# Kernel tuning notes

Hardware: AMD Instinct MI355X
Metric: run time of the kernel (lower is better)

Reference implementation:

```python
import jax, jax.numpy as jnp
import numpy as np
from jax import lax

DIM = 2048
NUM_HEADS = 16
HEAD_DIM = DIM // NUM_HEADS  # 128
BLOCK = 128
EPS = 1e-6


def setup_inputs() -> dict:
    key = jax.random.key(0)
    kq, kk, kv = jax.random.split(key, 3)
    B, S = 2, 4096
    q = jax.random.normal(kq, (B, S, DIM), dtype=jnp.float32)
    k = jax.random.normal(kk, (B, S, DIM), dtype=jnp.float32)
    v = jax.random.normal(kv, (B, S, DIM), dtype=jnp.float32)
    return {"q": q, "k": k, "v": v}


def _flash_attn(q, k, v):
    # q,k,v: [B, S, DIM] -> [B, H, S, Dh]
    B, S, _ = q.shape
    def split_heads(x):
        return jnp.transpose(x.reshape(B, -1, NUM_HEADS, HEAD_DIM), (0, 2, 1, 3))
    scale = HEAD_DIM ** (-0.5)
    qh = split_heads(q) * scale  # pre-scale, as in original __call__
    kh = split_heads(k)
    vh = split_heads(v)
    Sk = kh.shape[2]
    num_chunks = (Sk + BLOCK - 1) // BLOCK

    o0 = jnp.zeros((B, NUM_HEADS, S, HEAD_DIM), dtype=jnp.float32)
    l0 = jnp.zeros((B, NUM_HEADS, S, 1), dtype=jnp.float32)
    m0 = jnp.full((B, NUM_HEADS, S, 1), -jnp.inf, dtype=jnp.float32)

    def chunk_scanner(carry, chunk_idx):
        o, l, m_run = carry
        start = chunk_idx * BLOCK
        k_c = lax.dynamic_slice(kh, (0, 0, start, 0), (B, NUM_HEADS, BLOCK, HEAD_DIM))
        v_c = lax.dynamic_slice(vh, (0, 0, start, 0), (B, NUM_HEADS, BLOCK, HEAD_DIM))
        # scores: [B, H, Sq, BLOCK]; note second division by sqrt(head_dim) (faithful)
        s = jnp.einsum('bhqd,bhkd->bhqk', qh, k_c,
                       precision=lax.Precision.HIGHEST) / jnp.sqrt(jnp.float32(HEAD_DIM))
        m_chunk = jnp.max(s, axis=-1, keepdims=True)
        m_new = jnp.maximum(m_run, m_chunk)
        exp_scale = jnp.exp(m_run - m_new)
        exp_s = jnp.exp(s - m_chunk)  # faithful: uses m_chunk, not m_new
        l_new = l * exp_scale + jnp.sum(exp_s, axis=-1, keepdims=True)
        o_chunk = jnp.einsum('bhqk,bhkd->bhqd', exp_s, v_c,
                             precision=lax.Precision.HIGHEST)
        o_new = o * exp_scale + o_chunk
        return (o_new, l_new, m_new), None

    (o, l, _), _ = lax.scan(chunk_scanner, (o0, l0, m0), jnp.arange(num_chunks))
    o = o / (l + EPS)
    out = jnp.transpose(o, (0, 2, 1, 3)).reshape(B, -1, DIM)
    return out


def reference(q, k, v):
    return _flash_attn(q, k, v)
```

## Files before the change

kernel.cpp:

```cpp
#include <hip/hip_runtime.h>
#include <hip/hip_bf16.h>
#include <stdint.h>

#define SEQ     4096
#define DMODEL  2048
#define NHEADS  16
#define DHEAD   128
#define QBLK    256
#define CHUNK   128
#define NCHUNK  (SEQ / CHUNK)

typedef __bf16 bf16_t;
typedef bf16_t bf16x8 __attribute__((ext_vector_type(8)));
typedef bf16_t bf16x4 __attribute__((ext_vector_type(4)));
typedef float  f32x4  __attribute__((ext_vector_type(4)));

typedef __attribute__((address_space(3))) uint32_t       lds_u32_t;
typedef __attribute__((address_space(1))) const uint32_t glb_u32_t;

static __device__ __forceinline__ void gload16(const void* g, void* l) {
  __builtin_amdgcn_global_load_lds((glb_u32_t*)g, (lds_u32_t*)l, 16, 0, 0);
}

static __device__ __forceinline__ float exp2_fast(float x) {
  float r;
  asm("v_exp_f32 %0, %1\n\ts_nop 0" : "=v"(r) : "v"(x));
  return r;
}

__device__ __forceinline__ uint32_t swz(int row, int colbyte) {
  return ((uint32_t)(row * 256 + colbyte)) ^ ((uint32_t)(row & 15) << 4);
}

__global__ __launch_bounds__(256)
void prep_k(const float* __restrict__ kk, bf16_t* __restrict__ kb) {
  const size_t e = ((size_t)blockIdx.x * 256 + threadIdx.x) * 8;
  const int dm = (int)(e % DMODEL);
  const int s  = (int)((e / DMODEL) % SEQ);
  const int b  = (int)(e / ((size_t)DMODEL * SEQ));
  float4 x0 = *(const float4*)(kk + e);
  float4 x1 = *(const float4*)(kk + e + 4);
  bf16x8 y;
  y[0]=(bf16_t)x0.x; y[1]=(bf16_t)x0.y; y[2]=(bf16_t)x0.z; y[3]=(bf16_t)x0.w;
  y[4]=(bf16_t)x1.x; y[5]=(bf16_t)x1.y; y[6]=(bf16_t)x1.z; y[7]=(bf16_t)x1.w;
  const size_t out = (((size_t)(b * NHEADS + (dm >> 7)) * SEQ + s) << 7) + (dm & 127);
  *(bf16x8*)(kb + out) = y;
}

__global__ __launch_bounds__(256)
void prep_v(const float* __restrict__ vv, bf16_t* __restrict__ vb) {
  __shared__ bf16_t T[128 * 132];
  const int t = threadIdx.x;
  const int s0 = blockIdx.x * 128, h = blockIdx.y, b = blockIdx.z;
  const float* src = vv + ((size_t)(b * SEQ + s0)) * DMODEL + h * DHEAD;
#pragma unroll
  for (int p = 0; p < 16; ++p) {
    const int sr = p * 8 + (t >> 5), c4 = (t & 31) * 4;
    float4 x = *(const float4*)(src + (size_t)sr * DMODEL + c4);
    bf16_t* d = T + sr * 132 + c4;
    d[0]=(bf16_t)x.x; d[1]=(bf16_t)x.y; d[2]=(bf16_t)x.z; d[3]=(bf16_t)x.w;
  }
  __syncthreads();
  bf16_t* out = vb + ((size_t)(b * NHEADS + h)) * DHEAD * SEQ;
#pragma unroll
  for (int p = 0; p < 8; ++p) {
    const int d = p * 16 + (t >> 4), sc8 = (t & 15) * 8;
    bf16x8 y;
#pragma unroll
    for (int j = 0; j < 8; ++j) y[j] = T[(sc8 + j) * 132 + d];
    *(bf16x8*)(out + (size_t)d * SEQ + s0 + sc8) = y;
  }
}

__global__ __launch_bounds__(512, 1)
void fa_fwd_p(const float* __restrict__ qg, const bf16_t* __restrict__ kbg,
              const bf16_t* __restrict__ vbg, float* __restrict__ og)
{
  __shared__ char smem[65536];

  const int tid  = threadIdx.x;
  const int wave = tid >> 6;
  const int lane = tid & 63;
  const int l15  = lane & 15;
  const int lhi  = lane >> 4;

  const int nwg = gridDim.x * gridDim.y * gridDim.z;
  const int lin = blockIdx.x + gridDim.x * (blockIdx.y + gridDim.y * blockIdx.z);
  const int wg  = (lin % 8) * (nwg / 8) + lin / 8;
  const int bx  = wg % gridDim.x;
  const int h   = (wg / gridDim.x) % NHEADS;
  const int b   = wg / (gridDim.x * NHEADS);
  const int bh  = b * NHEADS + h;
  const int qrow0 = bx * QBLK + wave * 32;

  const bf16_t* kcb = kbg + ((size_t)bh * SEQ) * DHEAD;
  const bf16_t* vcb = vbg + ((size_t)bh * DHEAD) * SEQ;

#define ISSUE_K(koff, key0)                                                    \
  {                                                                            \
    _Pragma("unroll")                                                          \
    for (int u = 0; u < 2; ++u) {                                              \
      const int row = u * 32 + wave * 4 + (lane >> 4);                         \
      const int gx  = (row & 3) | (((row >> 3) & 3) << 2);                     \
      gload16(kcb + (size_t)((key0) + row) * 128 + (((lane & 15) ^ gx) * 8),   \
              smem + (koff) + u * 8192 + wave * 1024);                         \
    }                                                                          \
  }
#define ISSUE_V(key0)                                                          \
  {                                                                            \
    _Pragma("unroll")                                                          \
    for (int u = 0; u < 4; ++u) {                                              \
      const int dh = u * 32 + wave * 4 + (lane >> 4);                          \
      gload16(vcb + (size_t)dh * SEQ + (key0) + (((lane & 15) ^ (dh & 15)) * 8),\
              smem + 32768 + u * 8192 + wave * 1024);                          \
    }                                                                          \
  }

  ISSUE_K(0, 0);
  ISSUE_K(16384, 64);
  ISSUE_V(0);

  bf16x8 qa[8];
  {
    const float sc = 1.4426950408889634f / 128.0f;
#pragma unroll
    for (int h2 = 0; h2 < 2; ++h2) {
      const float* qp =
          qg + ((size_t)(b * SEQ + qrow0 + h2 * 16 + l15)) * DMODEL + h * DHEAD;
#pragma unroll
      for (int kb = 0; kb < 4; ++kb) {
        const float* p8 = qp + kb * 32 + lhi * 8;
        float4 x0 = *(const float4*)p8;
        float4 x1 = *(const float4*)(p8 + 4);
        bf16x8 a;
        a[0] = (bf16_t)(x0.x * sc); a[1] = (bf16_t)(x0.y * sc);
        a[2] = (bf16_t)(x0.z * sc); a[3] = (bf16_t)(x0.w * sc);
        a[4] = (bf16_t)(x1.x * sc); a[5] = (bf16_t)(x1.y * sc);
        a[6] = (bf16_t)(x1.z * sc); a[7] = (bf16_t)(x1.w * sc);
        qa[h2 * 4 + kb] = a;
      }
    }
  }

  f32x4 oacc[16];
#pragma unroll
  for (int nt = 0; nt < 16; ++nt) { f32x4 z = {0.f,0.f,0.f,0.f}; oacc[nt] = z; }
  float m_run0 = -INFINITY, l_run0 = 0.f;
  float m_run1 = -INFINITY, l_run1 = 0.f;

  asm volatile("s_waitcnt vmcnt(4)\n\ts_barrier" ::: "memory");

  for (int c = 0; c < NCHUNK; ++c) {
    f32x4 s0[8], s1[8];
    __builtin_amdgcn_s_setprio(1);
#pragma unroll
    for (int t = 0; t < 2; ++t) {
      const char* Kt = smem + t * 16384;
#pragma unroll
      for (int nl = 0; nl < 4; ++nl) {
        const int rowA = (nl >> 1) * 32 + (l15 >> 2) * 8 + (nl & 1) * 4 + (l15 & 3);
        const int gx   = (rowA & 3) | (((rowA >> 3) & 3) << 2);
        f32x4 a0 = {0.f, 0.f, 0.f, 0.f};
        f32x4 a1 = {0.f, 0.f, 0.f, 0.f};
#pragma unroll
        for (int j = 0; j < 4; ++j) {
          const uint32_t byte = (uint32_t)(rowA * 256) + ((j * 64 + lhi * 16) ^ (gx << 4));
          bf16x8 kf = *(const bf16x8*)(Kt + byte);
          a0 = __builtin_amdgcn_mfma_f32_16x16x32_bf16(kf, qa[j], a0, 0, 0, 0);
          a1 = __builtin_amdgcn_mfma_f32_16x16x32_bf16(kf, qa[4 + j], a1, 0, 0, 0);
        }
        s0[t * 4 + nl] = a0;
        s1[t * 4 + nl] = a1;
      }
    }
    __builtin_amdgcn_s_setprio(0);

    asm volatile("s_waitcnt vmcnt(0) lgkmcnt(0)\n\ts_barrier" ::: "memory");
    if (c + 1 < NCHUNK) {
      ISSUE_K(0, (c + 1) * CHUNK);
      ISSUE_K(16384, (c + 1) * CHUNK + 64);
    }

    bf16x8 pa0[4], pa1[4];
#define SOFTMAX_HALF(SA, PA, MRUN, LRUN, OBASE)                                \
    {                                                                          \
      float mc = SA[0][0];                                                     \
      _Pragma("unroll")                                                        \
      for (int i = 0; i < 8; ++i)                                              \
        _Pragma("unroll")                                                      \
        for (int r = 0; r < 4; ++r)                                            \
          if (i + r) mc = fmaxf(mc, SA[i][r]);                                 \
      mc = fmaxf(mc, __shfl_xor(mc, 16, 64));                                  \
      mc = fmaxf(mc, __shfl_xor(mc, 32, 64));                                  \
      const bool skip = __all(mc <= MRUN);                                     \
      const float mn = fmaxf(MRUN, mc);                                        \
      const float e  = exp2_fast(MRUN - mn);                                   \
      MRUN = mn;                                                               \
      float ps = 0.f;                                                          \
      _Pragma("unroll")                                                        \
      for (int nt = 0; nt < 8; ++nt)                                           \
        _Pragma("unroll")                                                      \
        for (int r = 0; r < 4; ++r) {                                          \
          const float p = exp2_fast(SA[nt][r] - mc);                           \
          ps += p;                                                             \
          PA[(nt >> 2) * 2 + ((nt >> 1) & 1)][(nt & 1) * 4 + r] = (bf16_t)p;   \
        }                                                                      \
      ps += __shfl_xor(ps, 16, 64);                                            \
      ps += __shfl_xor(ps, 32, 64);                                            \
      if (skip) {                                                              \
        LRUN += ps;                                                            \
      } else {                                                                 \
        LRUN = LRUN * e + ps;                                                  \
        _Pragma("unroll")                                                      \
        for (int r = 0; r < 4; ++r) {                                          \
          const float er = __shfl(e, lhi * 4 + r, 16);                         \
          _Pragma("unroll")                                                    \
          for (int nt = 0; nt < 8; ++nt) oacc[(OBASE) + nt][r] *= er;          \
        }                                                                      \
      }                                                                        \
    }
    SOFTMAX_HALF(s0, pa0, m_run0, l_run0, 0)
    SOFTMAX_HALF(s1, pa1, m_run1, l_run1, 8)
#undef SOFTMAX_HALF

    __builtin_amdgcn_s_setprio(1);
#pragma unroll
    for (int kv = 0; kv < 4; ++kv) {
#pragma unroll
      for (int nt = 0; nt < 8; ++nt) {
        const int dh = nt * 16 + l15;
        const uint32_t byte = (uint32_t)(32768 + dh * 256) +
            (((uint32_t)(kv * 64 + lhi * 16)) ^ ((dh & 15) << 4));
        bf16x8 vf = *(const bf16x8*)(smem + byte);
        oacc[nt]     = __builtin_amdgcn_mfma_f32_16x16x32_bf16(pa0[kv], vf, oacc[nt], 0, 0, 0);
        oacc[8 + nt] = __builtin_amdgcn_mfma_f32_16x16x32_bf16(pa1[kv], vf, oacc[8 + nt], 0, 0, 0);
      }
    }
    __builtin_amdgcn_s_setprio(0);

    asm volatile("s_waitcnt vmcnt(0) lgkmcnt(0)\n\ts_barrier" ::: "memory");
    if (c + 1 < NCHUNK) ISSUE_V((c + 1) * CHUNK);
  }

  {
    char* Ow = smem + wave * 8192;
#pragma unroll
    for (int h2 = 0; h2 < 2; ++h2) {
      const float lrl = h2 ? l_run1 : l_run0;
      float lr[4];
#pragma unroll
      for (int r = 0; r < 4; ++r) lr[r] = __shfl(lrl, lhi * 4 + r, 16);
#pragma unroll
      for (int nt = 0; nt < 8; ++nt)
#pragma unroll
        for (int r = 0; r < 4; ++r) {
          const int row = lhi * 4 + r;
          const int colb = (nt * 16 + l15) * 4;
          *(float*)(Ow + row * 512 + (colb ^ ((row & 7) << 4))) =
              oacc[h2 * 8 + nt][r] / (lr[r] + 1e-6f);
        }
      asm volatile("s_waitcnt lgkmcnt(0)" ::: "memory");
      __builtin_amdgcn_sched_barrier(0);
#pragma unroll
      for (int p = 0; p < 8; ++p) {
        const int row = p * 2 + (lane >> 5);
        const int colb = (lane & 31) * 16;
        f32x4 val = *(const f32x4*)(Ow + row * 512 + (colb ^ ((row & 7) << 4)));
        *(f32x4*)((char*)(og + ((size_t)(b * SEQ + qrow0 + h2 * 16 + row)) * DMODEL +
                          h * DHEAD) + colb) = val;
      }
      asm volatile("s_waitcnt lgkmcnt(0)" ::: "memory");
      __builtin_amdgcn_sched_barrier(0);
    }
  }
#undef ISSUE_K
#undef ISSUE_V
}

__global__ __launch_bounds__(512, 2)
void fa_fwd_raw(const float* __restrict__ qg, const float* __restrict__ kg,
                const float* __restrict__ vg, float* __restrict__ og)
{
  __shared__ bf16_t Kl[CHUNK * DHEAD];
  __shared__ bf16_t Vt[DHEAD * CHUNK];
  const int tid = threadIdx.x, wave = tid >> 6, lane = tid & 63;
  const int l15 = lane & 15, lhi = lane >> 4;
  const int b = blockIdx.z, h = blockIdx.y;
  const int qrow0 = blockIdx.x * 128 + wave * 16;
  bf16x8 qa[4];
  {
    const float* qp = qg + ((size_t)(b * SEQ + qrow0 + l15)) * DMODEL + h * DHEAD;
    const float sc = 1.0f / 128.0f;
#pragma unroll
    for (int kb = 0; kb < 4; ++kb) {
      const float* p8 = qp + kb * 32 + lhi * 8;
      float4 x0 = *(const float4*)p8; float4 x1 = *(const float4*)(p8 + 4);
      bf16x8 a;
      a[0]=(bf16_t)(x0.x*sc); a[1]=(bf16_t)(x0.y*sc); a[2]=(bf16_t)(x0.z*sc); a[3]=(bf16_t)(x0.w*sc);
      a[4]=(bf16_t)(x1.x*sc); a[5]=(bf16_t)(x1.y*sc); a[6]=(bf16_t)(x1.z*sc); a[7]=(bf16_t)(x1.w*sc);
      qa[kb] = a;
    }
  }
  f32x4 oacc[8];
#pragma unroll
  for (int nt = 0; nt < 8; ++nt) { f32x4 z = {0.f,0.f,0.f,0.f}; oacc[nt] = z; }
  float m_run[4] = {-INFINITY,-INFINITY,-INFINITY,-INFINITY};
  float l_run[4] = {0.f,0.f,0.f,0.f};
  const float* kbp = kg + ((size_t)b * SEQ) * DMODEL + h * DHEAD;
  const float* vbp = vg + ((size_t)b * SEQ) * DMODEL + h * DHEAD;
  const int krow16 = tid >> 5, kc4 = (tid & 31) * 4;
  const int vdh = tid & 127, vkg = (tid >> 7) * 8;
  for (int c = 0; c < NCHUNK; ++c) {
    const int key0 = c * CHUNK;
#pragma unroll
    for (int pass = 0; pass < 8; ++pass) {
      const int key = pass * 16 + krow16;
      const float4 x = *(const float4*)(kbp + (size_t)(key0 + key) * DMODEL + kc4);
      bf16x4 y; y[0]=(bf16_t)x.x; y[1]=(bf16_t)x.y; y[2]=(bf16_t)x.z; y[3]=(bf16_t)x.w;
      *(bf16x4*)((char*)Kl + swz(key, kc4 * 2)) = y;
    }
#pragma unroll
    for (int it = 0; it < 4; ++it) {
      const int kb0 = it * 32 + vkg;
      const float* vp = vbp + (size_t)(key0 + kb0) * DMODEL + vdh;
      bf16x8 y;
#pragma unroll
      for (int j = 0; j < 8; ++j) y[j] = (bf16_t)vp[(size_t)j * DMODEL];
      *(bf16x8*)((char*)Vt + swz(vdh, kb0 * 2)) = y;
    }
    __syncthreads();
    f32x4 sacc[8];
#pragma unroll
    for (int nt = 0; nt < 8; ++nt) {
      f32x4 acc = {0.f,0.f,0.f,0.f};
      const int key = nt * 16 + l15;
#pragma unroll
      for (int kb = 0; kb < 4; ++kb) {
        bf16x8 bfr = *(const bf16x8*)((const char*)Kl + swz(key, (kb*32+lhi*8)*2));
        acc = __builtin_amdgcn_mfma_f32_16x16x32_bf16(qa[kb], bfr, acc, 0, 0, 0);
      }
      sacc[nt] = acc;
    }
    __syncthreads();
    float mc[4];
#pragma unroll
    for (int r = 0; r < 4; ++r) {
      float m0 = sacc[0][r];
#pragma unroll
      for (int nt = 1; nt < 8; ++nt) m0 = fmaxf(m0, sacc[nt][r]);
      mc[r] = m0;
    }
#pragma unroll
    for (int sh = 1; sh < 16; sh <<= 1)
#pragma unroll
      for (int r = 0; r < 4; ++r) mc[r] = fmaxf(mc[r], __shfl_xor(mc[r], sh, 64));
    float esc[4], psum[4];
#pragma unroll
    for (int r = 0; r < 4; ++r) {
      const float mn = fmaxf(m_run[r], mc[r]);
      esc[r] = __expf(m_run[r] - mn); m_run[r] = mn; psum[r] = 0.f;
    }
    bf16_t* Pw = Kl + wave * (16 * 128);
#pragma unroll
    for (int nt = 0; nt < 8; ++nt)
#pragma unroll
      for (int r = 0; r < 4; ++r) {
        const float p = __expf(sacc[nt][r] - mc[r]);
        psum[r] += p;
        const int row = lhi * 4 + r;
        *(bf16_t*)((char*)Pw + swz(row, (nt*16+l15)*2)) = (bf16_t)p;
      }
#pragma unroll
    for (int sh = 1; sh < 16; sh <<= 1)
#pragma unroll
      for (int r = 0; r < 4; ++r) psum[r] += __shfl_xor(psum[r], sh, 64);
#pragma unroll
    for (int r = 0; r < 4; ++r) l_run[r] = l_run[r] * esc[r] + psum[r];
#pragma unroll
    for (int nt = 0; nt < 8; ++nt) {
      f32x4 o = oacc[nt];
      o[0]*=esc[0]; o[1]*=esc[1]; o[2]*=esc[2]; o[3]*=esc[3];
      oacc[nt] = o;
    }
    asm volatile("s_waitcnt lgkmcnt(0)" ::: "memory");
    __builtin_amdgcn_sched_barrier(0);
#pragma unroll
    for (int kb = 0; kb < 4; ++kb) {
      bf16x8 pf = *(const bf16x8*)((const char*)Pw + swz(l15, (kb*32+lhi*8)*2));
#pragma unroll
      for (int nt = 0; nt < 8; ++nt) {
        const int dh = nt * 16 + l15;
        bf16x8 vf = *(const bf16x8*)((const char*)Vt + swz(dh, (kb*32+lhi*8)*2));
        oacc[nt] = __builtin_amdgcn_mfma_f32_16x16x32_bf16(pf, vf, oacc[nt], 0, 0, 0);
      }
    }
    __syncthreads();
  }
#pragma unroll
  for (int nt = 0; nt < 8; ++nt)
#pragma unroll
    for (int r = 0; r < 4; ++r) {
      const int row = lhi * 4 + r;
      og[((size_t)(b * SEQ + qrow0 + row)) * DMODEL + h * DHEAD + nt * 16 + l15] =
          oacc[nt][r] / (l_run[r] + 1e-6f);
    }
}

extern "C" void kernel_launch(void* const* d_in, const int* in_sizes, int n_in,
                              void* d_out, int out_size, void* d_ws, size_t ws_size,
                              hipStream_t stream) {
  const float* q = (const float*)d_in[0];
  const float* k = (const float*)d_in[1];
  const float* v = (const float*)d_in[2];
  float* o = (float*)d_out;
  const int B = in_sizes[0] / (SEQ * DMODEL);
  const size_t kv_bytes = (size_t)B * NHEADS * SEQ * DHEAD * 2;
  if (ws_size >= 2 * kv_bytes) {
    bf16_t* kb = (bf16_t*)d_ws;
    bf16_t* vb = (bf16_t*)((char*)d_ws + kv_bytes);
    const int nthr = (int)(((size_t)B * SEQ * DMODEL) / 8);
    prep_k<<<nthr / 256, 256, 0, stream>>>(k, kb);
    dim3 gv(SEQ / 128, NHEADS, B);
    prep_v<<<gv, 256, 0, stream>>>(v, vb);
    dim3 grid(SEQ / QBLK, NHEADS, B);
    fa_fwd_p<<<grid, 512, 0, stream>>>(q, kb, vb, o);
  } else {
    dim3 grid(SEQ / 128, NHEADS, B);
    fa_fwd_raw<<<grid, 512, 0, stream>>>(q, k, v, o);
  }
}
```

Measured before the change: 335.7 us.

## Software-pipeline QK of next chunk with softmax/PV of current chunk, double-buffer K

Double-buffers the K tile in LDS (raising shared memory to 96KB) and restructures the main loop so the QK^T MFMAs for chunk c+1 are issued before the softmax and PV of chunk c, with K loads prefetched two chunks ahead. Score registers are ping-ponged between two sets. This aims to overlap exp/reduction VALU work with MFMA work and hide load latency. It also vectorises the row-max and row-sum reductions into trees. The cost is doubled score register pressure, which risks spills, and a larger LDS footprint per workgroup.

```diff
diff --git a/kernel.cpp b/kernel.cpp
--- a/kernel.cpp
+++ b/kernel.cpp
@@ -25,6 +25,13 @@
 static __device__ __forceinline__ float exp2_fast(float x) {
   float r;
   asm("v_exp_f32 %0, %1\n\ts_nop 0" : "=v"(r) : "v"(x));
+  return r;
+}
+
+static __device__ __forceinline__ f32x4 vmax4(f32x4 a, f32x4 b) {
+  f32x4 r;
+  r[0] = fmaxf(a[0], b[0]); r[1] = fmaxf(a[1], b[1]);
+  r[2] = fmaxf(a[2], b[2]); r[3] = fmaxf(a[3], b[3]);
   return r;
 }
 
@@ -76,7 +83,7 @@
 void fa_fwd_p(const float* __restrict__ qg, const bf16_t* __restrict__ kbg,
               const bf16_t* __restrict__ vbg, float* __restrict__ og)
 {
-  __shared__ char smem[65536];
+  __shared__ char smem[98304];
 
   const int tid  = threadIdx.x;
   const int wave = tid >> 6;
@@ -99,7 +106,7 @@
 #define ISSUE_K(koff, key0)                                                    \
   {                                                                            \
     _Pragma("unroll")                                                          \
-    for (int u = 0; u < 2; ++u) {                                              \
+    for (int u = 0; u < 4; ++u) {                                              \
       const int row = u * 32 + wave * 4 + (lane >> 4);                         \
       const int gx  = (row & 3) | (((row >> 3) & 3) << 2);                     \
       gload16(kcb + (size_t)((key0) + row) * 128 + (((lane & 15) ^ gx) * 8),   \
@@ -112,13 +119,9 @@
     for (int u = 0; u < 4; ++u) {                                              \
       const int dh = u * 32 + wave * 4 + (lane >> 4);                          \
       gload16(vcb + (size_t)dh * SEQ + (key0) + (((lane & 15) ^ (dh & 15)) * 8),\
-              smem + 32768 + u * 8192 + wave * 1024);                          \
+              smem + 65536 + u * 8192 + wave * 1024);                          \
     }                                                                          \
   }
-
-  ISSUE_K(0, 0);
-  ISSUE_K(16384, 64);
-  ISSUE_V(0);
 
   bf16x8 qa[8];
   {
@@ -142,69 +145,58 @@
     }
   }
 
-  f32x4 oacc[16];
-#pragma unroll
-  for (int nt = 0; nt < 16; ++nt) { f32x4 z = {0.f,0.f,0.f,0.f}; oacc[nt] = z; }
-  float m_run0 = -INFINITY, l_run0 = 0.f;
-  float m_run1 = -INFINITY, l_run1 = 0.f;
-
-  asm volatile("s_waitcnt vmcnt(4)\n\ts_barrier" ::: "memory");
-
-  for (int c = 0; c < NCHUNK; ++c) {
-    f32x4 s0[8], s1[8];
-    __builtin_amdgcn_s_setprio(1);
-#pragma unroll
-    for (int t = 0; t < 2; ++t) {
-      const char* Kt = smem + t * 16384;
-#pragma unroll
-      for (int nl = 0; nl < 4; ++nl) {
-        const int rowA = (nl >> 1) * 32 + (l15 >> 2) * 8 + (nl & 1) * 4 + (l15 & 3);
-        const int gx   = (rowA & 3) | (((rowA >> 3) & 3) << 2);
-        f32x4 a0 = {0.f, 0.f, 0.f, 0.f};
-        f32x4 a1 = {0.f, 0.f, 0.f, 0.f};
-#pragma unroll
-        for (int j = 0; j < 4; ++j) {
-          const uint32_t byte = (uint32_t)(rowA * 256) + ((j * 64 + lhi * 16) ^ (gx << 4));
-          bf16x8 kf = *(const bf16x8*)(Kt + byte);
-          a0 = __builtin_amdgcn_mfma_f32_16x16x32_bf16(kf, qa[j], a0, 0, 0, 0);
-          a1 = __builtin_amdgcn_mfma_f32_16x16x32_bf16(kf, qa[4 + j], a1, 0, 0, 0);
-        }
-        s0[t * 4 + nl] = a0;
-        s1[t * 4 + nl] = a1;
-      }
-    }
-    __builtin_amdgcn_s_setprio(0);
-
-    asm volatile("s_waitcnt vmcnt(0) lgkmcnt(0)\n\ts_barrier" ::: "memory");
-    if (c + 1 < NCHUNK) {
-      ISSUE_K(0, (c + 1) * CHUNK);
-      ISSUE_K(16384, (c + 1) * CHUNK + 64);
-    }
-
-    bf16x8 pa0[4], pa1[4];
+#define QK_STEP(S0A, S1A, KOFF)                                                \
+  {                                                                            \
+    __builtin_amdgcn_s_setprio(1);                                             \
+    _Pragma("unroll")                                                          \
+    for (int t = 0; t < 2; ++t) {                                              \
+      const char* Kt = smem + (KOFF) + t * 16384;                              \
+      _Pragma("unroll")                                                        \
+      for (int nl = 0; nl < 4; ++nl) {                                         \
+        const int rowA = (nl >> 1) * 32 + (l15 >> 2) * 8 + (nl & 1) * 4 + (l15 & 3); \
+        const int gx   = (rowA & 3) | (((rowA >> 3) & 3) << 2);                \
+        f32x4 a0 = {0.f, 0.f, 0.f, 0.f};                                       \
+        f32x4 a1 = {0.f, 0.f, 0.f, 0.f};                                       \
+        _Pragma("unroll")                                                      \
+        for (int j = 0; j < 4; ++j) {                                          \
+          const uint32_t byte = (uint32_t)(rowA * 256) +                       \
+                                ((j * 64 + lhi * 16) ^ (gx << 4));             \
+          bf16x8 kf = *(const bf16x8*)(Kt + byte);                             \
+          a0 = __builtin_amdgcn_mfma_f32_16x16x32_bf16(kf, qa[j], a0, 0, 0, 0);\
+          a1 = __builtin_amdgcn_mfma_f32_16x16x32_bf16(kf, qa[4 + j], a1, 0, 0, 0);\
+        }                                                                      \
+        S0A[t * 4 + nl] = a0;                                                  \
+        S1A[t * 4 + nl] = a1;                                                  \
+      }                                                                        \
+    }                                                                          \
+    __builtin_amdgcn_s_setprio(0);                                             \
+  }
+
 #define SOFTMAX_HALF(SA, PA, MRUN, LRUN, OBASE)                                \
     {                                                                          \
-      float mc = SA[0][0];                                                     \
-      _Pragma("unroll")                                                        \
-      for (int i = 0; i < 8; ++i)                                              \
-        _Pragma("unroll")                                                      \
-        for (int r = 0; r < 4; ++r)                                            \
-          if (i + r) mc = fmaxf(mc, SA[i][r]);                                 \
+      f32x4 t0 = vmax4(SA[0], SA[1]), t1 = vmax4(SA[2], SA[3]);                \
+      f32x4 t2 = vmax4(SA[4], SA[5]), t3 = vmax4(SA[6], SA[7]);                \
+      f32x4 t4 = vmax4(vmax4(t0, t1), vmax4(t2, t3));                          \
+      float mc = fmaxf(fmaxf(fmaxf(t4[0], t4[1]), t4[2]), t4[3]);              \
       mc = fmaxf(mc, __shfl_xor(mc, 16, 64));                                  \
       mc = fmaxf(mc, __shfl_xor(mc, 32, 64));                                  \
       const bool skip = __all(mc <= MRUN);                                     \
       const float mn = fmaxf(MRUN, mc);                                        \
       const float e  = exp2_fast(MRUN - mn);                                   \
       MRUN = mn;                                                               \
-      float ps = 0.f;                                                          \
+      f32x4 pe[8];                                                             \
       _Pragma("unroll")                                                        \
       for (int nt = 0; nt < 8; ++nt)                                           \
         _Pragma("unroll")                                                      \
         for (int r = 0; r < 4; ++r) {                                          \
           const float p = exp2_fast(SA[nt][r] - mc);                           \
-          ps += p;                                                             \
+          pe[nt][r] = p;                                                       \
           PA[(nt >> 2) * 2 + ((nt >> 1) & 1)][(nt & 1) * 4 + r] = (bf16_t)p;   \
         }                                                                      \
+      f32x4 q0 = pe[0] + pe[1], q1 = pe[2] + pe[3];                            \
+      f32x4 q2 = pe[4] + pe[5], q3 = pe[6] + pe[7];                            \
+      f32x4 q4 = (q0 + q1) + (q2 + q3);                                        \
+      float ps = (q4[0] + q4[1]) + (q4[2] + q4[3]);                            \
       ps += __shfl_xor(ps, 16, 64);                                            \
       ps += __shfl_xor(ps, 32, 64);                                            \
       if (skip) {                                                              \
@@ -219,27 +211,55 @@
         }                                                                      \
       }                                                                        \
     }
-    SOFTMAX_HALF(s0, pa0, m_run0, l_run0, 0)
-    SOFTMAX_HALF(s1, pa1, m_run1, l_run1, 8)
-#undef SOFTMAX_HALF
-
-    __builtin_amdgcn_s_setprio(1);
-#pragma unroll
-    for (int kv = 0; kv < 4; ++kv) {
-#pragma unroll
-      for (int nt = 0; nt < 8; ++nt) {
-        const int dh = nt * 16 + l15;
-        const uint32_t byte = (uint32_t)(32768 + dh * 256) +
-            (((uint32_t)(kv * 64 + lhi * 16)) ^ ((dh & 15) << 4));
-        bf16x8 vf = *(const bf16x8*)(smem + byte);
-        oacc[nt]     = __builtin_amdgcn_mfma_f32_16x16x32_bf16(pa0[kv], vf, oacc[nt], 0, 0, 0);
-        oacc[8 + nt] = __builtin_amdgcn_mfma_f32_16x16x32_bf16(pa1[kv], vf, oacc[8 + nt], 0, 0, 0);
-      }
-    }
-    __builtin_amdgcn_s_setprio(0);
-
-    asm volatile("s_waitcnt vmcnt(0) lgkmcnt(0)\n\ts_barrier" ::: "memory");
-    if (c + 1 < NCHUNK) ISSUE_V((c + 1) * CHUNK);
+
+#define PV_STEP()                                                              \
+  {                                                                            \
+    __builtin_amdgcn_s_setprio(1);                                             \
+    _Pragma("unroll")                                                          \
+    for (int kv = 0; kv < 4; ++kv) {                                           \
+      _Pragma("unroll")                                                        \
+      for (int nt = 0; nt < 8; ++nt) {                                         \
+        const int dh = nt * 16 + l15;                                          \
+        const uint32_t byte = (uint32_t)(65536 + dh * 256) +                   \
+            (((uint32_t)(kv * 64 + lhi * 16)) ^ ((dh & 15) << 4));             \
+        bf16x8 vf = *(const bf16x8*)(smem + byte);                             \
+        oacc[nt]     = __builtin_amdgcn_mfma_f32_16x16x32_bf16(pa0[kv], vf, oacc[nt], 0, 0, 0);      \
+        oacc[8 + nt] = __builtin_amdgcn_mfma_f32_16x16x32_bf16(pa1[kv], vf, oacc[8 + nt], 0, 0, 0);  \
+      }                                                                        \
+    }                                                                          \
+    __builtin_amdgcn_s_setprio(0);                                             \
+  }
+
+#define PIPE_ITER(c, SC0, SC1, SN0, SN1, KNEXT_OFF, KSTAGE_OFF)                \
+  {                                                                            \
+    asm volatile("s_waitcnt vmcnt(0)\n\ts_barrier" ::: "memory");              \
+    if ((c) + 1 < NCHUNK) QK_STEP(SN0, SN1, KNEXT_OFF);                        \
+    bf16x8 pa0[4], pa1[4];                                                     \
+    SOFTMAX_HALF(SC0, pa0, m_run0, l_run0, 0)                                  \
+    SOFTMAX_HALF(SC1, pa1, m_run1, l_run1, 8)                                  \
+    PV_STEP();                                                                 \
+    asm volatile("s_waitcnt lgkmcnt(0)\n\ts_barrier" ::: "memory");            \
+    if ((c) + 2 < NCHUNK) ISSUE_K(KSTAGE_OFF, ((c) + 2) * CHUNK);              \
+    if ((c) + 1 < NCHUNK) ISSUE_V(((c) + 1) * CHUNK);                          \
+  }
+
+  f32x4 oacc[16];
+#pragma unroll
+  for (int nt = 0; nt < 16; ++nt) { f32x4 z = {0.f,0.f,0.f,0.f}; oacc[nt] = z; }
+  float m_run0 = -INFINITY, l_run0 = 0.f;
+  float m_run1 = -INFINITY, l_run1 = 0.f;
+
+  f32x4 sA0[8], sA1[8], sB0[8], sB1[8];
+
+  ISSUE_K(0, 0);
+  ISSUE_V(0);
+  asm volatile("s_waitcnt vmcnt(4)\n\ts_barrier" ::: "memory");
+  ISSUE_K(32768, CHUNK);
+  QK_STEP(sA0, sA1, 0);
+
+  for (int c = 0; c < NCHUNK; c += 2) {
+    PIPE_ITER(c,     sA0, sA1, sB0, sB1, 32768, 0);
+    PIPE_ITER(c + 1, sB0, sB1, sA0, sA1, 0,     32768);
   }
 
   {
@@ -273,6 +293,10 @@
       __builtin_amdgcn_sched_barrier(0);
     }
   }
+#undef PIPE_ITER
+#undef PV_STEP
+#undef SOFTMAX_HALF
+#undef QK_STEP
 #undef ISSUE_K
 #undef ISSUE_V
 }
```

Result: slower. 1.213 ms (+261.3%).
